# Optimization experiments

Measured on AMD Instinct MI355X. Metric: run time of the kernel, lower is better.

The kernel has to match this reference:

```python
import jax, jax.numpy as jnp
import numpy as np

NEG_SLOPE = 0.2  # PyG GATConv default negative_slope


def gat_conv(x, src, dst, W, a_src, a_dst, bias, concat=True):
    """PyG-style GATConv (self-loops already appended to src/dst).
    x: [N, Fin], W: [Fin, H*C], a_src/a_dst: [H, C], bias: [H*C] or [C].
    """
    N = x.shape[0]
    H, C = a_src.shape
    h = (x @ W).reshape(N, H, C)                       # [N, H, C]
    s_src = jnp.einsum('nhc,hc->nh', h, a_src)         # per-node src logit
    s_dst = jnp.einsum('nhc,hc->nh', h, a_dst)         # per-node dst logit
    e = jax.nn.leaky_relu(s_src[src] + s_dst[dst], NEG_SLOPE)   # [E, H]
    # segment softmax over incoming edges of each destination node
    m = jax.ops.segment_max(e, dst, num_segments=N)    # [N, H]
    ex = jnp.exp(e - m[dst])
    denom = jax.ops.segment_sum(ex, dst, num_segments=N)
    alpha = ex / (denom[dst] + 1e-16)                  # [E, H]
    out = jax.ops.segment_sum(h[src] * alpha[:, :, None], dst, num_segments=N)  # [N,H,C]
    out = out.reshape(N, H * C) if concat else out.mean(axis=1)
    return out + bias


def setup_inputs() -> dict:
    key = jax.random.key(0)
    ks = jax.random.split(key, 12)
    N, E = 20000, 320000
    Fin, Hd, Hh = 384, 256, 4
    x = jax.random.normal(ks[0], (N, Fin), dtype=jnp.float32)
    edge_index = jax.random.randint(ks[1], (2, E), 0, N, dtype=jnp.int32)
    s = lambda k, shp, fan: jax.random.normal(k, shp, dtype=jnp.float32) / np.sqrt(fan)
    return {
        'x': x, 'edge_index': edge_index,
        'W1': s(ks[2], (Fin, Hh * Hd), Fin),
        'a_src1': s(ks[3], (Hh, Hd), Hd), 'a_dst1': s(ks[4], (Hh, Hd), Hd),
        'b1': jnp.zeros((Hh * Hd,), jnp.float32),
        'W2': s(ks[5], (Hh * Hd, Hd), Hh * Hd),
        'a_src2': s(ks[6], (1, Hd), Hd), 'a_dst2': s(ks[7], (1, Hd), Hd),
        'b2': jnp.zeros((Hd,), jnp.float32),
        'Wp1': s(ks[8], (Hd, Hd // 2), Hd), 'bp1': jnp.zeros((Hd // 2,), jnp.float32),
        'Wp2': s(ks[9], (Hd // 2, 1), Hd // 2), 'bp2': jnp.zeros((1,), jnp.float32),
    }


def reference(x, edge_index, W1, a_src1, a_dst1, b1, W2, a_src2, a_dst2, b2,
              Wp1, bp1, Wp2, bp2):
    N = x.shape[0]
    loops = jnp.arange(N, dtype=edge_index.dtype)
    src = jnp.concatenate([edge_index[0], loops])  # PyG add_self_loops=True
    dst = jnp.concatenate([edge_index[1], loops])
    h = jax.nn.elu(gat_conv(x, src, dst, W1, a_src1, a_dst1, b1, concat=True))
    h = jax.nn.elu(gat_conv(h, src, dst, W2, a_src2, a_dst2, b2, concat=True))
    graph_features = jnp.mean(h, axis=0, keepdims=True)  # batch=None path
    infl = jax.nn.sigmoid(jax.nn.relu(h @ Wp1 + bp1) @ Wp2 + bp2)
    return h, graph_features, infl
```

## Files before the change

### kernel.cpp

```cpp
#include <hip/hip_runtime.h>

#define NEG_SLOPE 0.2f
#define SM_SHIFT 3.0f

typedef __bf16 bf16x8 __attribute__((ext_vector_type(8)));
typedef float floatx4 __attribute__((ext_vector_type(4)));
typedef float floatx2 __attribute__((ext_vector_type(2)));
typedef unsigned short ushortx4 __attribute__((ext_vector_type(4)));
typedef unsigned short ushortx8 __attribute__((ext_vector_type(8)));

__device__ __forceinline__ float eluf(float x) { return x > 0.f ? x : __expf(x) - 1.f; }
__device__ __forceinline__ float lrelu(float x) { return x > 0.f ? x : NEG_SLOPE * x; }

__device__ __forceinline__ unsigned short f2bf(float f) {
    unsigned u = __float_as_uint(f);
    u += 0x7FFFu + ((u >> 16) & 1u);
    return (unsigned short)(u >> 16);
}
__device__ __forceinline__ float bf2f(unsigned short h) {
    return __uint_as_float(((unsigned)h) << 16);
}
__device__ __forceinline__ floatx2 mk2(unsigned u) {
    floatx2 r;
    r.x = __uint_as_float(u << 16);
    r.y = __uint_as_float(u & 0xFFFF0000u);
    return r;
}

__device__ __forceinline__ void async16(const unsigned short* g, unsigned short* l) {
    __builtin_amdgcn_global_load_lds(
        (const __attribute__((address_space(1))) unsigned int*)g,
        (__attribute__((address_space(3))) unsigned int*)l,
        16, 0, 0);
}

__global__ __launch_bounds__(256) void prep_kernel(
        const int* __restrict__ ei, int E, int N, int* __restrict__ counts,
        const float* __restrict__ x, unsigned short* __restrict__ xb,
        const float* __restrict__ W1, unsigned short* __restrict__ w1t,
        const float* __restrict__ W2, unsigned short* __restrict__ w2t,
        const float* __restrict__ Wp1, unsigned short* __restrict__ wp1t,
        const float* __restrict__ as1, const float* __restrict__ ad1, float* __restrict__ U) {
    __shared__ float tile[32][33];
    int b = blockIdx.x;
    int t = threadIdx.x;
    int Et = E + N;
    int nA = (Et + 255) >> 8;
    int nB = (N * 96 + 255) >> 8;
    if (b < nA) {
        int i = b * 256 + t;
        if (i < Et) {
            int d = (i < E) ? ei[E + i] : (i - E);
            atomicAdd(&counts[d], 1);
        }
    } else if (b < nA + nB) {
        int i = (b - nA) * 256 + t;
        if (i < N * 96) {
            float4 v = ((const float4*)x)[i];
            ushortx4 o;
            o[0] = f2bf(v.x); o[1] = f2bf(v.y); o[2] = f2bf(v.z); o[3] = f2bf(v.w);
            *(ushortx4*)(xb + (size_t)i * 4) = o;
        }
    } else if (b < nA + nB + 384) {
        int idx = b - nA - nB;
        int n0 = (idx & 31) * 32, k0 = (idx >> 5) * 32;
        int tx = t & 31, ty = t >> 5;
        #pragma unroll
        for (int i = 0; i < 32; i += 8)
            tile[ty + i][tx] = W1[(size_t)(k0 + ty + i) * 1024 + n0 + tx];
        __syncthreads();
        #pragma unroll
        for (int i = 0; i < 32; i += 8)
            w1t[(size_t)(n0 + ty + i) * 384 + k0 + tx] = f2bf(tile[tx][ty + i]);
    } else if (b < nA + nB + 384 + 256) {
        int idx = b - nA - nB - 384;
        int n0 = (idx & 7) * 32, k0 = (idx >> 3) * 32;
        int tx = t & 31, ty = t >> 5;
        #pragma unroll
        for (int i = 0; i < 32; i += 8)
            tile[ty + i][tx] = W2[(size_t)(k0 + ty + i) * 256 + n0 + tx];
        __syncthreads();
        #pragma unroll
        for (int i = 0; i < 32; i += 8)
            w2t[(size_t)(n0 + ty + i) * 1024 + k0 + tx] = f2bf(tile[tx][ty + i]);
    } else if (b < nA + nB + 384 + 256 + 32) {
        int idx = b - nA - nB - 384 - 256;
        int n0 = (idx & 3) * 32, k0 = (idx >> 2) * 32;
        int tx = t & 31, ty = t >> 5;
        #pragma unroll
        for (int i = 0; i < 32; i += 8)
            tile[ty + i][tx] = Wp1[(size_t)(k0 + ty + i) * 128 + n0 + tx];
        __syncthreads();
        #pragma unroll
        for (int i = 0; i < 32; i += 8)
            wp1t[(size_t)(n0 + ty + i) * 256 + k0 + tx] = f2bf(tile[tx][ty + i]);
    } else {
        int idx = b - nA - nB - 384 - 256 - 32;
        int k = idx * 4 + (t >> 6);
        int lane = t & 63;
        #pragma unroll
        for (int r = 0; r < 8; r++) {
            int h = r & 3;
            const float* a = (r < 4 ? as1 : ad1) + h * 256 + lane * 4;
            const float* w = W1 + (size_t)k * 1024 + h * 256 + lane * 4;
            float4 wv = *(const float4*)w;
            float4 av = *(const float4*)a;
            float p = wv.x * av.x + wv.y * av.y + wv.z * av.z + wv.w * av.w;
            #pragma unroll
            for (int off = 32; off; off >>= 1) p += __shfl_xor(p, off);
            if (lane == 0) U[r * 384 + k] = p;
        }
    }
}

__global__ void scan_kernel(int* __restrict__ counts_cursor, int* __restrict__ row_ptr, int N) {
    __shared__ int s_wsum[16];
    __shared__ int s_carry;
    int t = threadIdx.x;
    int lane = t & 63, wid = t >> 6;
    if (t == 0) { s_carry = 0; row_ptr[0] = 0; }
    __syncthreads();
    for (int start = 0; start < N; start += 1024) {
        int i = start + t;
        int v = (i < N) ? counts_cursor[i] : 0;
        int s = v;
        #pragma unroll
        for (int d = 1; d < 64; d <<= 1) {
            int u = __shfl_up(s, d);
            if (lane >= d) s += u;
        }
        if (lane == 63) s_wsum[wid] = s;
        __syncthreads();
        if (wid == 0) {
            int w = (lane < 16) ? s_wsum[lane] : 0;
            #pragma unroll
            for (int d = 1; d < 16; d <<= 1) {
                int u = __shfl_up(w, d);
                if (lane >= d) w += u;
            }
            if (lane < 16) s_wsum[lane] = w;
        }
        __syncthreads();
        int incl = s + (wid ? s_wsum[wid - 1] : 0) + s_carry;
        if (i < N) { row_ptr[i + 1] = incl; counts_cursor[i] = incl - v; }
        __syncthreads();
        if (t == 0) s_carry += s_wsum[15];
        __syncthreads();
    }
}

__global__ void fill_kernel(const int* __restrict__ ei, int E, int N,
                            int* __restrict__ cursor, int* __restrict__ col) {
    int i = blockIdx.x * blockDim.x + threadIdx.x;
    int Et = E + N;
    if (i >= Et) return;
    int s, d;
    if (i < E) { s = ei[i]; d = ei[E + i]; } else { s = d = i - E; }
    int pos = atomicAdd(&cursor[d], 1);
    col[pos] = s;
}

__global__ void sU_kernel(const unsigned short* __restrict__ xb, const float* __restrict__ U,
                          float* __restrict__ ss1, float* __restrict__ sd1, int N) {
    int wid = (blockIdx.x * blockDim.x + threadIdx.x) >> 6;
    int lane = threadIdx.x & 63;
    if (wid >= N) return;
    int half = lane >> 5, l32 = lane & 31;
    int c0 = l32 * 12;
    const unsigned short* row = xb + (size_t)wid * 384 + c0;
    ushortx8 v8 = *(const ushortx8*)row;
    ushortx4 v4 = *(const ushortx4*)(row + 8);
    float xv[12];
    #pragma unroll
    for (int j = 0; j < 8; j++) xv[j] = bf2f(v8[j]);
    #pragma unroll
    for (int j = 0; j < 4; j++) xv[8 + j] = bf2f(v4[j]);
    float p[4];
    #pragma unroll
    for (int r = 0; r < 4; r++) {
        const float* u = U + (half * 4 + r) * 384 + c0;
        float s = 0.f;
        #pragma unroll
        for (int j = 0; j < 12; j++) s += xv[j] * u[j];
        #pragma unroll
        for (int off = 16; off; off >>= 1) s += __shfl_xor(s, off);
        p[r] = s;
    }
    if (l32 == 0) {
        float* dst = half ? (sd1 + wid * 4) : (ss1 + wid * 4);
        dst[0] = p[0]; dst[1] = p[1]; dst[2] = p[2]; dst[3] = p[3];
    }
}

__global__ void s2_kernel(const unsigned short* __restrict__ h2b, const float* __restrict__ a_src,
                          const float* __restrict__ a_dst, float* __restrict__ ssrc,
                          float* __restrict__ sdst, int N) {
    int wid = (blockIdx.x * blockDim.x + threadIdx.x) >> 6;
    int lane = threadIdx.x & 63;
    if (wid >= N) return;
    ushortx4 v = *(const ushortx4*)(h2b + (size_t)wid * 256 + lane * 4);
    float4 a = ((const float4*)a_src)[lane];
    float4 d = ((const float4*)a_dst)[lane];
    float v0 = bf2f(v[0]), v1 = bf2f(v[1]), v2 = bf2f(v[2]), v3 = bf2f(v[3]);
    float s = v0 * a.x + v1 * a.y + v2 * a.z + v3 * a.w;
    float t = v0 * d.x + v1 * d.y + v2 * d.z + v3 * d.w;
    for (int off = 32; off; off >>= 1) { s += __shfl_xor(s, off); t += __shfl_xor(t, off); }
    if (lane == 0) { ssrc[wid] = s; sdst[wid] = t; }
}

__global__ __launch_bounds__(256) void aggx_kernel(const unsigned short* __restrict__ xb,
        const float* __restrict__ ss1, const float* __restrict__ sd1,
        const int* __restrict__ row_ptr, const int* __restrict__ col,
        unsigned short* __restrict__ aggxn, int N) {
    __shared__ unsigned short lds[4][1536];
    __shared__ float pipe[4][72][8];
    int t = threadIdx.x;
    int wv = t >> 6;
    int wid = blockIdx.x * 4 + wv;
    int lane = t & 63;
    bool active = wid < N;
    int half = lane >> 5, l32 = lane & 31;
    int c0 = l32 * 12;
    float4 dsum = {0.f, 0.f, 0.f, 0.f};
    floatx2 acc2[4][6] = {};
    if (active) {
        if (lane < 8) {
            float* pz = &pipe[wv][64 + lane][0];
            #pragma unroll
            for (int j = 0; j < 8; j++) pz[j] = 0.f;
        }
        int base = row_ptr[wid];
        int deg = row_ptr[wid + 1] - base;
        float4 sd = *(const float4*)(sd1 + (size_t)wid * 4);
        for (int chunk = 0; chunk < deg; chunk += 64) {
            int cnt = min(64, deg - chunk);
            int cl = chunk + lane;
            int myO = 0;
            float4 myW = {0.f, 0.f, 0.f, 0.f};
            if (cl < deg) {
                int s = col[base + cl];
                float4 sp = *(const float4*)(ss1 + (size_t)s * 4);
                myW.x = __expf(lrelu(sp.x + sd.x) - SM_SHIFT); dsum.x += myW.x;
                myW.y = __expf(lrelu(sp.y + sd.y) - SM_SHIFT); dsum.y += myW.y;
                myW.z = __expf(lrelu(sp.z + sd.z) - SM_SHIFT); dsum.z += myW.z;
                myW.w = __expf(lrelu(sp.w + sd.w) - SM_SHIFT); dsum.w += myW.w;
                myO = s * 384;
            }
            float* pe = &pipe[wv][lane][0];
            *(float4*)pe = myW;
            pe[4] = __int_as_float(myO);
            int K = (cnt + 1) >> 1;
#define LOADSTG(wS, u4_, u2_, stg) { \
            const float* pq = &pipe[wv][(stg) * 2 + half][0]; \
            wS = *(const float4*)pq; \
            int oN = __float_as_int(pq[4]); \
            const unsigned short* rN = xb + (unsigned)(oN + c0); \
            u4_ = *(const uint4*)rN; u2_ = *(const uint2*)(rN + 8); }
#define CONSUME(cw, u4_, u2_) { \
            floatx2 xv[6]; \
            xv[0] = mk2(u4_.x); xv[1] = mk2(u4_.y); xv[2] = mk2(u4_.z); \
            xv[3] = mk2(u4_.w); xv[4] = mk2(u2_.x); xv[5] = mk2(u2_.y); \
            _Pragma("unroll") for (int j2 = 0; j2 < 6; j2++) { \
                acc2[0][j2] += cw.x * xv[j2]; \
                acc2[1][j2] += cw.y * xv[j2]; \
                acc2[2][j2] += cw.z * xv[j2]; \
                acc2[3][j2] += cw.w * xv[j2]; } }
            float4 wA, wB, wC, wD;
            uint4 uA4, uB4, uC4, uD4;
            uint2 uA2, uB2, uC2, uD2;
            LOADSTG(wA, uA4, uA2, 0)
            LOADSTG(wB, uB4, uB2, 1)
            LOADSTG(wC, uC4, uC2, 2)
            LOADSTG(wD, uD4, uD2, 3)
            int k = 0;
            for (; k + 4 <= K; k += 4) {
                { float4 cw = wA; uint4 u4 = uA4; uint2 u2 = uA2;
                  LOADSTG(wA, uA4, uA2, k + 4) CONSUME(cw, u4, u2) }
                { float4 cw = wB; uint4 u4 = uB4; uint2 u2 = uB2;
                  LOADSTG(wB, uB4, uB2, k + 5) CONSUME(cw, u4, u2) }
                { float4 cw = wC; uint4 u4 = uC4; uint2 u2 = uC2;
                  LOADSTG(wC, uC4, uC2, k + 6) CONSUME(cw, u4, u2) }
                { float4 cw = wD; uint4 u4 = uD4; uint2 u2 = uD2;
                  LOADSTG(wD, uD4, uD2, k + 7) CONSUME(cw, u4, u2) }
            }
            if (k < K)     { CONSUME(wA, uA4, uA2) }
            if (k + 1 < K) { CONSUME(wB, uB4, uB2) }
            if (k + 2 < K) { CONSUME(wC, uC4, uC2) }
#undef LOADSTG
#undef CONSUME
        }
        #pragma unroll
        for (int off = 32; off; off >>= 1) {
            dsum.x += __shfl_xor(dsum.x, off);
            dsum.y += __shfl_xor(dsum.y, off);
            dsum.z += __shfl_xor(dsum.z, off);
            dsum.w += __shfl_xor(dsum.w, off);
        }
        #pragma unroll
        for (int h = 0; h < 4; h++)
            #pragma unroll
            for (int j2 = 0; j2 < 6; j2++) {
                acc2[h][j2].x += __shfl_xor(acc2[h][j2].x, 32);
                acc2[h][j2].y += __shfl_xor(acc2[h][j2].y, 32);
            }
        float dsel0 = half ? dsum.z : dsum.x;
        float dsel1 = half ? dsum.w : dsum.y;
        #pragma unroll
        for (int hh = 0; hh < 2; hh++) {
            int h = half * 2 + hh;
            float dh = hh ? dsel1 : dsel0;
            float inv = 1.f / (dh + 1e-16f);
            ushortx8 o8; ushortx4 o4;
            #pragma unroll
            for (int j = 0; j < 8; j++) {
                float v = half ? acc2[2 + hh][j >> 1][j & 1] : acc2[hh][j >> 1][j & 1];
                o8[j] = f2bf(v * inv);
            }
            #pragma unroll
            for (int j = 0; j < 4; j++) {
                int jj = 8 + j;
                float v = half ? acc2[2 + hh][jj >> 1][jj & 1] : acc2[hh][jj >> 1][jj & 1];
                o4[j] = f2bf(v * inv);
            }
            unsigned short* lp = &lds[wv][h * 384 + c0];
            *(ushortx8*)lp = o8;
            *(ushortx4*)(lp + 8) = o4;
        }
    }
    __syncthreads();
    size_t blockBase = (size_t)blockIdx.x * 4 * 1536;
    const unsigned short* lflat = &lds[0][0];
    #pragma unroll
    for (int j = 0; j < 3; j++) {
        int so = j * 2048 + t * 8;
        int node = blockIdx.x * 4 + so / 1536;
        if (node < N)
            *(ushortx8*)(aggxn + blockBase + so) = *(const ushortx8*)(lflat + so);
    }
}

#define LDK 40

__global__ __launch_bounds__(256) void gemm_l1(const unsigned short* __restrict__ A,
        const unsigned short* __restrict__ Bt, const float* __restrict__ bias,
        unsigned short* __restrict__ Cout, int M) {
    __shared__ unsigned short As[2][128 * 32];
    __shared__ unsigned short Bs[2][128 * 32];
    int t = threadIdx.x;
    int lane = t & 63, wave = t >> 6;
    int wm = (wave >> 1) * 64, wn = (wave & 1) * 64;
    int q = lane >> 4, l16 = lane & 15;
    int row0 = blockIdx.y * 128, col0 = blockIdx.x * 128;
    int hoff = (col0 >> 8) * 384;
    floatx4 acc[4][4] = {};
    int srow = t >> 2, skc = (t & 3) * 8;
    const unsigned short* Ag0 = A + (size_t)min(row0 + srow, M - 1) * 1536 + hoff + skc;
    const unsigned short* Ag1 = A + (size_t)min(row0 + srow + 64, M - 1) * 1536 + hoff + skc;
    const unsigned short* Bg0 = Bt + (size_t)(col0 + srow) * 384 + skc;
    const unsigned short* Bg1 = Bt + (size_t)(col0 + srow + 64) * 384 + skc;
#define STG_L1(buf, kt) \
    async16(Ag0 + (kt), &As[buf][t * 8]); \
    async16(Ag1 + (kt), &As[buf][2048 + t * 8]); \
    async16(Bg0 + (kt), &Bs[buf][t * 8]); \
    async16(Bg1 + (kt), &Bs[buf][2048 + t * 8]);
    STG_L1(0, 0)
    __syncthreads();
    #pragma unroll
    for (int ti = 0; ti < 12; ++ti) {
        int cur = ti & 1;
        if (ti < 11) { STG_L1(cur ^ 1, (ti + 1) * 32) }
        __builtin_amdgcn_sched_barrier(0);
        bf16x8 af[4], bfr[4];
        #pragma unroll
        for (int i = 0; i < 4; i++)
            af[i] = *(const bf16x8*)&As[cur][(wm + i * 16 + l16) * 32 + q * 8];
        #pragma unroll
        for (int j = 0; j < 4; j++)
            bfr[j] = *(const bf16x8*)&Bs[cur][(wn + j * 16 + l16) * 32 + q * 8];
        #pragma unroll
        for (int i = 0; i < 4; i++)
            #pragma unroll
            for (int j = 0; j < 4; j++)
                acc[i][j] = __builtin_amdgcn_mfma_f32_16x16x32_bf16(af[i], bfr[j], acc[i][j], 0, 0, 0);
        __syncthreads();
    }
#undef STG_L1
    float bj[4];
    #pragma unroll
    for (int j = 0; j < 4; j++) bj[j] = bias[col0 + wn + l16 + j * 16];
    #pragma unroll
    for (int i = 0; i < 4; i++) {
        #pragma unroll
        for (int r = 0; r < 4; r++) {
            int grow = row0 + wm + i * 16 + q * 4 + r;
            if (grow < M) {
                unsigned short* cp = Cout + (size_t)grow * 1024 + col0 + wn + l16;
                #pragma unroll
                for (int j = 0; j < 4; j++) cp[j * 16] = f2bf(eluf(acc[i][j][r] + bj[j]));
            }
        }
    }
}

__global__ __launch_bounds__(256) void gemm_l2(const unsigned short* __restrict__ A,
        const unsigned short* __restrict__ Bt, unsigned short* __restrict__ Cout, int M) {
    __shared__ unsigned short As[2][128 * 32];
    __shared__ unsigned short Bs[2][64 * 32];
    int t = threadIdx.x;
    int lane = t & 63, wave = t >> 6;
    int wm = (wave >> 1) * 64, wn = (wave & 1) * 32;
    int q = lane >> 4, l16 = lane & 15;
    int row0 = blockIdx.y * 128, col0 = blockIdx.x * 64;
    floatx4 acc[4][2] = {};
    int srow = t >> 2, skc = (t & 3) * 8;
    const unsigned short* Ag0 = A + (size_t)min(row0 + srow, M - 1) * 1024 + skc;
    const unsigned short* Ag1 = A + (size_t)min(row0 + srow + 64, M - 1) * 1024 + skc;
    const unsigned short* Bg0 = Bt + (size_t)(col0 + srow) * 1024 + skc;
#define STG_L2(buf, kt) \
    async16(Ag0 + (kt), &As[buf][t * 8]); \
    async16(Ag1 + (kt), &As[buf][2048 + t * 8]); \
    async16(Bg0 + (kt), &Bs[buf][t * 8]);
    STG_L2(0, 0)
    __syncthreads();
    #pragma unroll
    for (int ti = 0; ti < 32; ++ti) {
        int cur = ti & 1;
        if (ti < 31) { STG_L2(cur ^ 1, (ti + 1) * 32) }
        __builtin_amdgcn_sched_barrier(0);
        bf16x8 af[4], bfr[2];
        #pragma unroll
        for (int i = 0; i < 4; i++)
            af[i] = *(const bf16x8*)&As[cur][(wm + i * 16 + l16) * 32 + q * 8];
        #pragma unroll
        for (int j = 0; j < 2; j++)
            bfr[j] = *(const bf16x8*)&Bs[cur][(wn + j * 16 + l16) * 32 + q * 8];
        #pragma unroll
        for (int i = 0; i < 4; i++)
            #pragma unroll
            for (int j = 0; j < 2; j++)
                acc[i][j] = __builtin_amdgcn_mfma_f32_16x16x32_bf16(af[i], bfr[j], acc[i][j], 0, 0, 0);
        __syncthreads();
    }
#undef STG_L2
    #pragma unroll
    for (int i = 0; i < 4; i++) {
        #pragma unroll
        for (int r = 0; r < 4; r++) {
            int grow = row0 + wm + i * 16 + q * 4 + r;
            if (grow < M) {
                unsigned short* cp = Cout + (size_t)grow * 256 + col0 + wn + l16;
                #pragma unroll
                for (int j = 0; j < 2; j++) cp[j * 16] = f2bf(acc[i][j][r]);
            }
        }
    }
}

__global__ __launch_bounds__(256) void agg2_kernel(const unsigned short* __restrict__ h2b,
        const float* __restrict__ ss2, const float* __restrict__ sd2,
        const int* __restrict__ row_ptr, const int* __restrict__ col,
        const float* __restrict__ bias, float* __restrict__ out,
        unsigned short* __restrict__ outb, int N) {
    __shared__ float pipe2[4][76][2];
    int t = threadIdx.x;
    int wv = t >> 6;
    int wid = (blockIdx.x * blockDim.x + t) >> 6;
    int lane = t & 63;
    if (wid >= N) return;
    if (lane < 12) {
        pipe2[wv][64 + lane][0] = 0.f;
        pipe2[wv][64 + lane][1] = 0.f;
    }
    int base = row_ptr[wid];
    int deg = row_ptr[wid + 1] - base;
    float sd = sd2[wid];
    floatx2 accA = {0.f, 0.f}, accB = {0.f, 0.f};
    float dsum = 0.f;
    int ch = lane * 4;
    for (int chunk = 0; chunk < deg; chunk += 64) {
        int cnt = min(64, deg - chunk);
        int cl = chunk + lane;
        int myO = 0;
        float myW = 0.f;
        if (cl < deg) {
            int s = col[base + cl];
            myW = __expf(lrelu(ss2[s] + sd) - SM_SHIFT);
            dsum += myW;
            myO = s * 256;
        }
        pipe2[wv][lane][0] = myW;
        pipe2[wv][lane][1] = __int_as_float(myO);
        int K = (cnt + 1) >> 1;
#define LOADSTG2(w0_, w1_, u0_, u1_, stg) { \
        const float* q0 = &pipe2[wv][(stg) * 2][0]; \
        const float* q1 = &pipe2[wv][(stg) * 2 + 1][0]; \
        w0_ = q0[0]; int o0 = __float_as_int(q0[1]); \
        w1_ = q1[0]; int o1 = __float_as_int(q1[1]); \
        u0_ = *(const uint2*)(h2b + (unsigned)(o0 + ch)); \
        u1_ = *(const uint2*)(h2b + (unsigned)(o1 + ch)); }
#define CONSUME2(w0_, w1_, u0_, u1_) { \
        accA += w0_ * mk2(u0_.x); accA += w1_ * mk2(u1_.x); \
        accB += w0_ * mk2(u0_.y); accB += w1_ * mk2(u1_.y); }
        float wa0, wa1, wb0, wb1, wc0, wc1, wd0, wd1, we0, we1, wf0, wf1;
        uint2 ua0, ua1, ub0, ub1, uc0, uc1, ud0, ud1, ue0, ue1, uf0, uf1;
        LOADSTG2(wa0, wa1, ua0, ua1, 0)
        LOADSTG2(wb0, wb1, ub0, ub1, 1)
        LOADSTG2(wc0, wc1, uc0, uc1, 2)
        LOADSTG2(wd0, wd1, ud0, ud1, 3)
        LOADSTG2(we0, we1, ue0, ue1, 4)
        LOADSTG2(wf0, wf1, uf0, uf1, 5)
        int k = 0;
        for (; k + 6 <= K; k += 6) {
            { float p0 = wa0, p1 = wa1; uint2 v0 = ua0, v1 = ua1;
              LOADSTG2(wa0, wa1, ua0, ua1, k + 6) CONSUME2(p0, p1, v0, v1) }
            { float p0 = wb0, p1 = wb1; uint2 v0 = ub0, v1 = ub1;
              LOADSTG2(wb0, wb1, ub0, ub1, k + 7) CONSUME2(p0, p1, v0, v1) }
            { float p0 = wc0, p1 = wc1; uint2 v0 = uc0, v1 = uc1;
              LOADSTG2(wc0, wc1, uc0, uc1, k + 8) CONSUME2(p0, p1, v0, v1) }
            { float p0 = wd0, p1 = wd1; uint2 v0 = ud0, v1 = ud1;
              LOADSTG2(wd0, wd1, ud0, ud1, k + 9) CONSUME2(p0, p1, v0, v1) }
            { float p0 = we0, p1 = we1; uint2 v0 = ue0, v1 = ue1;
              LOADSTG2(we0, we1, ue0, ue1, k + 10) CONSUME2(p0, p1, v0, v1) }
            { float p0 = wf0, p1 = wf1; uint2 v0 = uf0, v1 = uf1;
              LOADSTG2(wf0, wf1, uf0, uf1, k + 11) CONSUME2(p0, p1, v0, v1) }
        }
        if (k < K)     { CONSUME2(wa0, wa1, ua0, ua1) }
        if (k + 1 < K) { CONSUME2(wb0, wb1, ub0, ub1) }
        if (k + 2 < K) { CONSUME2(wc0, wc1, uc0, uc1) }
        if (k + 3 < K) { CONSUME2(wd0, wd1, ud0, ud1) }
        if (k + 4 < K) { CONSUME2(we0, we1, ue0, ue1) }
#undef LOADSTG2
#undef CONSUME2
    }
    #pragma unroll
    for (int off = 32; off; off >>= 1) dsum += __shfl_xor(dsum, off);
    float inv = 1.f / (dsum + 1e-16f);
    float4 o;
    o.x = eluf(accA.x * inv + bias[ch + 0]);
    o.y = eluf(accA.y * inv + bias[ch + 1]);
    o.z = eluf(accB.x * inv + bias[ch + 2]);
    o.w = eluf(accB.y * inv + bias[ch + 3]);
    *(float4*)(out + (size_t)wid * 256 + ch) = o;
    ushortx4 ob;
    ob[0] = f2bf(o.x); ob[1] = f2bf(o.y); ob[2] = f2bf(o.z); ob[3] = f2bf(o.w);
    *(ushortx4*)(outb + (size_t)wid * 256 + ch) = ob;
}

__global__ __launch_bounds__(256) void tail_kernel(const float* __restrict__ h,
        const unsigned short* __restrict__ hbf, const unsigned short* __restrict__ wp1t,
        const float* __restrict__ bp1, const float* __restrict__ Wp2,
        const float* __restrict__ bp2, float* __restrict__ gf, float* __restrict__ infl, int M) {
    int b = blockIdx.x;
    int nInfl = (M + 127) / 128;
    if (b < nInfl) {
        __shared__ unsigned short As[128 * LDK];
        __shared__ unsigned short Bs[128 * LDK];
        __shared__ float partial[2][128];
        int t = threadIdx.x;
        int lane = t & 63, wave = t >> 6;
        int wm = (wave >> 1) * 64, wn = (wave & 1) * 64;
        int q = lane >> 4, l16 = lane & 15;
        int row0 = b * 128;
        floatx4 acc[4][4] = {};
        int sg = (t & 7) * 4;
        int sr = t >> 3;
        for (int kt = 0; kt < 256; kt += 32) {
            #pragma unroll
            for (int p = 0; p < 4; p++) {
                int r = sr + p * 32;
                int ga = min(row0 + r, M - 1);
                *(ushortx4*)&As[r * LDK + sg] = *(const ushortx4*)(hbf + (size_t)ga * 256 + kt + sg);
                *(ushortx4*)&Bs[r * LDK + sg] = *(const ushortx4*)(wp1t + (size_t)r * 256 + kt + sg);
            }
            __syncthreads();
            bf16x8 af[4], bfr[4];
            #pragma unroll
            for (int i = 0; i < 4; i++)
                af[i] = *(const bf16x8*)&As[(wm + i * 16 + l16) * LDK + q * 8];
            #pragma unroll
            for (int j = 0; j < 4; j++)
                bfr[j] = *(const bf16x8*)&Bs[(wn + j * 16 + l16) * LDK + q * 8];
            #pragma unroll
            for (int i = 0; i < 4; i++)
                #pragma unroll
                for (int j = 0; j < 4; j++)
                    acc[i][j] = __builtin_amdgcn_mfma_f32_16x16x32_bf16(af[i], bfr[j], acc[i][j], 0, 0, 0);
            __syncthreads();
        }
        float b1v[4], w2v[4];
        #pragma unroll
        for (int j = 0; j < 4; j++) {
            int colj = wn + j * 16 + l16;
            b1v[j] = bp1[colj];
            w2v[j] = Wp2[colj];
        }
        #pragma unroll
        for (int i = 0; i < 4; i++) {
            #pragma unroll
            for (int r = 0; r < 4; r++) {
                float s = fmaxf(acc[i][0][r] + b1v[0], 0.f) * w2v[0]
                        + fmaxf(acc[i][1][r] + b1v[1], 0.f) * w2v[1]
                        + fmaxf(acc[i][2][r] + b1v[2], 0.f) * w2v[2]
                        + fmaxf(acc[i][3][r] + b1v[3], 0.f) * w2v[3];
                #pragma unroll
                for (int off = 1; off < 16; off <<= 1) s += __shfl_xor(s, off);
                if (l16 == 0) partial[wave & 1][wm + i * 16 + q * 4 + r] = s;
            }
        }
        __syncthreads();
        if (t < 128) {
            int row = row0 + t;
            if (row < M) {
                float v = partial[0][t] + partial[1][t] + bp2[0];
                infl[row] = 1.f / (1.f + __expf(-v));
            }
        }
    } else {
        int bb = b - nInfl;
        int c = threadIdx.x;
        int per = (M + 159) / 160;
        int n0 = bb * per;
        int n1 = min(M, n0 + per);
        float a0 = 0.f, a1 = 0.f, a2 = 0.f, a3 = 0.f;
        float a4 = 0.f, a5 = 0.f, a6 = 0.f, a7 = 0.f;
        int n = n0;
        for (; n + 8 <= n1; n += 8) {
            a0 += h[(size_t)(n + 0) * 256 + c];
            a1 += h[(size_t)(n + 1) * 256 + c];
            a2 += h[(size_t)(n + 2) * 256 + c];
            a3 += h[(size_t)(n + 3) * 256 + c];
            a4 += h[(size_t)(n + 4) * 256 + c];
            a5 += h[(size_t)(n + 5) * 256 + c];
            a6 += h[(size_t)(n + 6) * 256 + c];
            a7 += h[(size_t)(n + 7) * 256 + c];
        }
        for (; n < n1; n++) a0 += h[(size_t)n * 256 + c];
        float acc = ((a0 + a1) + (a2 + a3)) + ((a4 + a5) + (a6 + a7));
        atomicAdd(&gf[c], acc * (1.0f / M));
    }
}

extern "C" void kernel_launch(void* const* d_in, const int* in_sizes, int n_in,
                              void* d_out, int out_size, void* d_ws, size_t ws_size,
                              hipStream_t stream) {
    const float* x   = (const float*)d_in[0];
    const int*   ei  = (const int*)d_in[1];
    const float* W1  = (const float*)d_in[2];
    const float* as1 = (const float*)d_in[3];
    const float* ad1 = (const float*)d_in[4];
    const float* b1  = (const float*)d_in[5];
    const float* W2  = (const float*)d_in[6];
    const float* as2 = (const float*)d_in[7];
    const float* ad2 = (const float*)d_in[8];
    const float* b2  = (const float*)d_in[9];
    const float* Wp1 = (const float*)d_in[10];
    const float* bp1 = (const float*)d_in[11];
    const float* Wp2 = (const float*)d_in[12];
    const float* bp2 = (const float*)d_in[13];

    const int N  = in_sizes[0] / 384;
    const int E  = in_sizes[1] / 2;
    const int Et = E + N;

    char* wsp = (char*)d_ws;
    unsigned short* xb    = (unsigned short*)wsp; wsp += (size_t)N * 384  * sizeof(short);
    unsigned short* aggxn = (unsigned short*)wsp; wsp += (size_t)N * 1536 * sizeof(short);
    unsigned short* h1eb  = (unsigned short*)wsp; wsp += (size_t)N * 1024 * sizeof(short);
    unsigned short* h2b   = (unsigned short*)wsp; wsp += (size_t)N * 256  * sizeof(short);
    unsigned short* hbf   = (unsigned short*)wsp; wsp += (size_t)N * 256  * sizeof(short);
    unsigned short* w1t   = (unsigned short*)wsp; wsp += (size_t)1024 * 384 * sizeof(short);
    unsigned short* w2t   = (unsigned short*)wsp; wsp += (size_t)256 * 1024 * sizeof(short);
    unsigned short* wp1t  = (unsigned short*)wsp; wsp += (size_t)128 * 256 * sizeof(short);
    float* U   = (float*)wsp; wsp += (size_t)8 * 384 * sizeof(float);
    float* ss1 = (float*)wsp; wsp += (size_t)N * 4 * sizeof(float);
    float* sd1 = (float*)wsp; wsp += (size_t)N * 4 * sizeof(float);
    float* ss2 = (float*)wsp; wsp += (size_t)N * sizeof(float);
    float* sd2 = (float*)wsp; wsp += (size_t)N * sizeof(float);
    int* row_ptr = (int*)wsp; wsp += (size_t)(N + 1) * sizeof(int);
    int* cursor  = (int*)wsp; wsp += (size_t)N * sizeof(int);
    int* col     = (int*)wsp;

    float* out_h  = (float*)d_out;
    float* out_gf = out_h + (size_t)N * 256;
    float* out_if = out_gf + 256;

    hipMemsetAsync(cursor, 0, (size_t)N * sizeof(int), stream);
    int nA = (Et + 255) / 256;
    int nB = (N * 96 + 255) / 256;
    int nPrep = nA + nB + 384 + 256 + 32 + 96;
    prep_kernel<<<nPrep, 256, 0, stream>>>(ei, E, N, cursor, x, xb, W1, w1t, W2, w2t, Wp1, wp1t, as1, ad1, U);
    scan_kernel<<<1, 1024, 0, stream>>>(cursor, row_ptr, N);
    fill_kernel<<<nA, 256, 0, stream>>>(ei, E, N, cursor, col);

    sU_kernel<<<(N + 3) / 4, 256, 0, stream>>>(xb, U, ss1, sd1, N);
    aggx_kernel<<<(N + 3) / 4, 256, 0, stream>>>(xb, ss1, sd1, row_ptr, col, aggxn, N);
    gemm_l1<<<dim3(8, (N + 127) / 128), 256, 0, stream>>>(aggxn, w1t, b1, h1eb, N);

    gemm_l2<<<dim3(4, (N + 127) / 128), 256, 0, stream>>>(h1eb, w2t, h2b, N);
    s2_kernel<<<(N + 3) / 4, 256, 0, stream>>>(h2b, as2, ad2, ss2, sd2, N);
    agg2_kernel<<<(N + 3) / 4, 256, 0, stream>>>(h2b, ss2, sd2, row_ptr, col, b2, out_h, hbf, N);

    hipMemsetAsync(out_gf, 0, 256 * sizeof(float), stream);
    tail_kernel<<<(N + 127) / 128 + 160, 256, 0, stream>>>(out_h, hbf, wp1t, bp1, Wp2, bp2, out_gf, out_if, N);
}
```

Baseline: 338.9 us.

## Fuse fill with sU, fold s2 logits into gemm_l2 epilogue, single-pass scan

Replaces the looped block scan with a single pass where each thread scans 20 counts serially. Merges the CSR fill and layer-1 logit kernels into one launch, and computes the layer-2 src/dst logits inside the gemm_l2 epilogue via shuffle reductions and atomics (with an added memset). The graph-mean reduction now reads the bf16 copy of h instead of fp32. This reduces launches and memory traffic. The scan now caps N at 20480 and the mean uses bf16-rounded values.

```diff
diff --git a/kernel.cpp b/kernel.cpp
--- a/kernel.cpp
+++ b/kernel.cpp
@@ -113,99 +113,97 @@
     }
 }
 
+#define SCAN_PER 20
 __global__ void scan_kernel(int* __restrict__ counts_cursor, int* __restrict__ row_ptr, int N) {
     __shared__ int s_wsum[16];
-    __shared__ int s_carry;
     int t = threadIdx.x;
     int lane = t & 63, wid = t >> 6;
-    if (t == 0) { s_carry = 0; row_ptr[0] = 0; }
+    int i0 = t * SCAN_PER;
+    int v[SCAN_PER];
+    int lsum = 0;
+    #pragma unroll
+    for (int j = 0; j < SCAN_PER; j++) {
+        int i = i0 + j;
+        int x = (i < N) ? counts_cursor[i] : 0;
+        v[j] = lsum;
+        lsum += x;
+    }
+    int s = lsum;
+    #pragma unroll
+    for (int d = 1; d < 64; d <<= 1) {
+        int u = __shfl_up(s, d);
+        if (lane >= d) s += u;
+    }
+    if (lane == 63) s_wsum[wid] = s;
     __syncthreads();
-    for (int start = 0; start < N; start += 1024) {
-        int i = start + t;
-        int v = (i < N) ? counts_cursor[i] : 0;
-        int s = v;
-        #pragma unroll
-        for (int d = 1; d < 64; d <<= 1) {
-            int u = __shfl_up(s, d);
-            if (lane >= d) s += u;
-        }
-        if (lane == 63) s_wsum[wid] = s;
-        __syncthreads();
-        if (wid == 0) {
-            int w = (lane < 16) ? s_wsum[lane] : 0;
-            #pragma unroll
-            for (int d = 1; d < 16; d <<= 1) {
-                int u = __shfl_up(w, d);
-                if (lane >= d) w += u;
-            }
-            if (lane < 16) s_wsum[lane] = w;
-        }
-        __syncthreads();
-        int incl = s + (wid ? s_wsum[wid - 1] : 0) + s_carry;
-        if (i < N) { row_ptr[i + 1] = incl; counts_cursor[i] = incl - v; }
-        __syncthreads();
-        if (t == 0) s_carry += s_wsum[15];
-        __syncthreads();
-    }
-}
-
-__global__ void fill_kernel(const int* __restrict__ ei, int E, int N,
-                            int* __restrict__ cursor, int* __restrict__ col) {
-    int i = blockIdx.x * blockDim.x + threadIdx.x;
+    if (wid == 0 && lane < 16) {
+        int w = s_wsum[lane];
+        #pragma unroll
+        for (int d = 1; d < 16; d <<= 1) {
+            int u = __shfl_up(w, d);
+            if (lane >= d) w += u;
+        }
+        s_wsum[lane] = w;
+    }
+    __syncthreads();
+    int base = s - lsum + (wid ? s_wsum[wid - 1] : 0);
+    if (t == 0) row_ptr[0] = 0;
+    #pragma unroll
+    for (int j = 0; j < SCAN_PER; j++) {
+        int i = i0 + j;
+        if (i < N) {
+            int excl = base + v[j];
+            int incl = base + ((j + 1 < SCAN_PER) ? v[j + 1] : lsum);
+            counts_cursor[i] = excl;
+            row_ptr[i + 1] = incl;
+        }
+    }
+}
+
+__global__ __launch_bounds__(256) void fill_sU_kernel(const int* __restrict__ ei, int E, int N,
+        int* __restrict__ cursor, int* __restrict__ col,
+        const unsigned short* __restrict__ xb, const float* __restrict__ U,
+        float* __restrict__ ss1, float* __restrict__ sd1) {
+    int b = blockIdx.x;
     int Et = E + N;
-    if (i >= Et) return;
-    int s, d;
-    if (i < E) { s = ei[i]; d = ei[E + i]; } else { s = d = i - E; }
-    int pos = atomicAdd(&cursor[d], 1);
-    col[pos] = s;
-}
-
-__global__ void sU_kernel(const unsigned short* __restrict__ xb, const float* __restrict__ U,
-                          float* __restrict__ ss1, float* __restrict__ sd1, int N) {
-    int wid = (blockIdx.x * blockDim.x + threadIdx.x) >> 6;
-    int lane = threadIdx.x & 63;
-    if (wid >= N) return;
-    int half = lane >> 5, l32 = lane & 31;
-    int c0 = l32 * 12;
-    const unsigned short* row = xb + (size_t)wid * 384 + c0;
-    ushortx8 v8 = *(const ushortx8*)row;
-    ushortx4 v4 = *(const ushortx4*)(row + 8);
-    float xv[12];
-    #pragma unroll
-    for (int j = 0; j < 8; j++) xv[j] = bf2f(v8[j]);
-    #pragma unroll
-    for (int j = 0; j < 4; j++) xv[8 + j] = bf2f(v4[j]);
-    float p[4];
-    #pragma unroll
-    for (int r = 0; r < 4; r++) {
-        const float* u = U + (half * 4 + r) * 384 + c0;
-        float s = 0.f;
-        #pragma unroll
-        for (int j = 0; j < 12; j++) s += xv[j] * u[j];
-        #pragma unroll
-        for (int off = 16; off; off >>= 1) s += __shfl_xor(s, off);
-        p[r] = s;
-    }
-    if (l32 == 0) {
-        float* dst = half ? (sd1 + wid * 4) : (ss1 + wid * 4);
-        dst[0] = p[0]; dst[1] = p[1]; dst[2] = p[2]; dst[3] = p[3];
-    }
-}
-
-__global__ void s2_kernel(const unsigned short* __restrict__ h2b, const float* __restrict__ a_src,
-                          const float* __restrict__ a_dst, float* __restrict__ ssrc,
-                          float* __restrict__ sdst, int N) {
-    int wid = (blockIdx.x * blockDim.x + threadIdx.x) >> 6;
-    int lane = threadIdx.x & 63;
-    if (wid >= N) return;
-    ushortx4 v = *(const ushortx4*)(h2b + (size_t)wid * 256 + lane * 4);
-    float4 a = ((const float4*)a_src)[lane];
-    float4 d = ((const float4*)a_dst)[lane];
-    float v0 = bf2f(v[0]), v1 = bf2f(v[1]), v2 = bf2f(v[2]), v3 = bf2f(v[3]);
-    float s = v0 * a.x + v1 * a.y + v2 * a.z + v3 * a.w;
-    float t = v0 * d.x + v1 * d.y + v2 * d.z + v3 * d.w;
-    for (int off = 32; off; off >>= 1) { s += __shfl_xor(s, off); t += __shfl_xor(t, off); }
-    if (lane == 0) { ssrc[wid] = s; sdst[wid] = t; }
+    int nF = (Et + 255) >> 8;
+    if (b < nF) {
+        int i = b * 256 + threadIdx.x;
+        if (i >= Et) return;
+        int s, d;
+        if (i < E) { s = ei[i]; d = ei[E + i]; } else { s = d = i - E; }
+        int pos = atomicAdd(&cursor[d], 1);
+        col[pos] = s;
+    } else {
+        int wid = ((b - nF) * 256 + threadIdx.x) >> 6;
+        int lane = threadIdx.x & 63;
+        if (wid >= N) return;
+        int half = lane >> 5, l32 = lane & 31;
+        int c0 = l32 * 12;
+        const unsigned short* row = xb + (size_t)wid * 384 + c0;
+        ushortx8 v8 = *(const ushortx8*)row;
+        ushortx4 v4 = *(const ushortx4*)(row + 8);
+        float xv[12];
+        #pragma unroll
+        for (int j = 0; j < 8; j++) xv[j] = bf2f(v8[j]);
+        #pragma unroll
+        for (int j = 0; j < 4; j++) xv[8 + j] = bf2f(v4[j]);
+        float p[4];
+        #pragma unroll
+        for (int r = 0; r < 4; r++) {
+            const float* u = U + (half * 4 + r) * 384 + c0;
+            float s = 0.f;
+            #pragma unroll
+            for (int j = 0; j < 12; j++) s += xv[j] * u[j];
+            #pragma unroll
+            for (int off = 16; off; off >>= 1) s += __shfl_xor(s, off);
+            p[r] = s;
+        }
+        if (l32 == 0) {
+            float* dst = half ? (sd1 + wid * 4) : (ss1 + wid * 4);
+            dst[0] = p[0]; dst[1] = p[1]; dst[2] = p[2]; dst[3] = p[3];
+        }
+    }
 }
 
 __global__ __launch_bounds__(256) void aggx_kernel(const unsigned short* __restrict__ xb,
@@ -403,7 +401,9 @@
 }
 
 __global__ __launch_bounds__(256) void gemm_l2(const unsigned short* __restrict__ A,
-        const unsigned short* __restrict__ Bt, unsigned short* __restrict__ Cout, int M) {
+        const unsigned short* __restrict__ Bt, const float* __restrict__ as2,
+        const float* __restrict__ ad2, unsigned short* __restrict__ Cout,
+        float* __restrict__ ssrc, float* __restrict__ sdst, int M) {
     __shared__ unsigned short As[2][128 * 32];
     __shared__ unsigned short Bs[2][64 * 32];
     int t = threadIdx.x;
@@ -442,15 +442,33 @@
         __syncthreads();
     }
 #undef STG_L2
+    float as2v[2], ad2v[2];
+    #pragma unroll
+    for (int j = 0; j < 2; j++) {
+        int colj = col0 + wn + l16 + j * 16;
+        as2v[j] = as2[colj];
+        ad2v[j] = ad2[colj];
+    }
     #pragma unroll
     for (int i = 0; i < 4; i++) {
         #pragma unroll
         for (int r = 0; r < 4; r++) {
             int grow = row0 + wm + i * 16 + q * 4 + r;
+            float ps = acc[i][0][r] * as2v[0] + acc[i][1][r] * as2v[1];
+            float pt = acc[i][0][r] * ad2v[0] + acc[i][1][r] * ad2v[1];
+            #pragma unroll
+            for (int off = 1; off < 16; off <<= 1) {
+                ps += __shfl_xor(ps, off);
+                pt += __shfl_xor(pt, off);
+            }
             if (grow < M) {
                 unsigned short* cp = Cout + (size_t)grow * 256 + col0 + wn + l16;
                 #pragma unroll
                 for (int j = 0; j < 2; j++) cp[j * 16] = f2bf(acc[i][j][r]);
+                if (l16 == 0) {
+                    atomicAdd(&ssrc[grow], ps);
+                    atomicAdd(&sdst[grow], pt);
+                }
             }
         }
     }
@@ -546,7 +564,7 @@
     *(ushortx4*)(outb + (size_t)wid * 256 + ch) = ob;
 }
 
-__global__ __launch_bounds__(256) void tail_kernel(const float* __restrict__ h,
+__global__ __launch_bounds__(256) void tail_kernel(
         const unsigned short* __restrict__ hbf, const unsigned short* __restrict__ wp1t,
         const float* __restrict__ bp1, const float* __restrict__ Wp2,
         const float* __restrict__ bp2, float* __restrict__ gf, float* __restrict__ infl, int M) {
@@ -625,16 +643,16 @@
         float a4 = 0.f, a5 = 0.f, a6 = 0.f, a7 = 0.f;
         int n = n0;
         for (; n + 8 <= n1; n += 8) {
-            a0 += h[(size_t)(n + 0) * 256 + c];
-            a1 += h[(size_t)(n + 1) * 256 + c];
-            a2 += h[(size_t)(n + 2) * 256 + c];
-            a3 += h[(size_t)(n + 3) * 256 + c];
-            a4 += h[(size_t)(n + 4) * 256 + c];
-            a5 += h[(size_t)(n + 5) * 256 + c];
-            a6 += h[(size_t)(n + 6) * 256 + c];
-            a7 += h[(size_t)(n + 7) * 256 + c];
-        }
-        for (; n < n1; n++) a0 += h[(size_t)n * 256 + c];
+            a0 += bf2f(hbf[(size_t)(n + 0) * 256 + c]);
+            a1 += bf2f(hbf[(size_t)(n + 1) * 256 + c]);
+            a2 += bf2f(hbf[(size_t)(n + 2) * 256 + c]);
+            a3 += bf2f(hbf[(size_t)(n + 3) * 256 + c]);
+            a4 += bf2f(hbf[(size_t)(n + 4) * 256 + c]);
+            a5 += bf2f(hbf[(size_t)(n + 5) * 256 + c]);
+            a6 += bf2f(hbf[(size_t)(n + 6) * 256 + c]);
+            a7 += bf2f(hbf[(size_t)(n + 7) * 256 + c]);
+        }
+        for (; n < n1; n++) a0 += bf2f(hbf[(size_t)n * 256 + c]);
         float acc = ((a0 + a1) + (a2 + a3)) + ((a4 + a5) + (a6 + a7));
         atomicAdd(&gf[c], acc * (1.0f / M));
     }
@@ -690,16 +708,15 @@
     int nPrep = nA + nB + 384 + 256 + 32 + 96;
     prep_kernel<<<nPrep, 256, 0, stream>>>(ei, E, N, cursor, x, xb, W1, w1t, W2, w2t, Wp1, wp1t, as1, ad1, U);
     scan_kernel<<<1, 1024, 0, stream>>>(cursor, row_ptr, N);
-    fill_kernel<<<nA, 256, 0, stream>>>(ei, E, N, cursor, col);
-
-    sU_kernel<<<(N + 3) / 4, 256, 0, stream>>>(xb, U, ss1, sd1, N);
+    fill_sU_kernel<<<nA + (N + 3) / 4, 256, 0, stream>>>(ei, E, N, cursor, col, xb, U, ss1, sd1);
+
     aggx_kernel<<<(N + 3) / 4, 256, 0, stream>>>(xb, ss1, sd1, row_ptr, col, aggxn, N);
     gemm_l1<<<dim3(8, (N + 127) / 128), 256, 0, stream>>>(aggxn, w1t, b1, h1eb, N);
 
-    gemm_l2<<<dim3(4, (N + 127) / 128), 256, 0, stream>>>(h1eb, w2t, h2b, N);
-    s2_kernel<<<(N + 3) / 4, 256, 0, stream>>>(h2b, as2, ad2, ss2, sd2, N);
+    hipMemsetAsync(ss2, 0, (size_t)2 * N * sizeof(float), stream);
+    gemm_l2<<<dim3(4, (N + 127) / 128), 256, 0, stream>>>(h1eb, w2t, as2, ad2, h2b, ss2, sd2, N);
     agg2_kernel<<<(N + 3) / 4, 256, 0, stream>>>(h2b, ss2, sd2, row_ptr, col, b2, out_h, hbf, N);
 
     hipMemsetAsync(out_gf, 0, 256 * sizeof(float), stream);
-    tail_kernel<<<(N + 127) / 128 + 160, 256, 0, stream>>>(out_h, hbf, wp1t, bp1, Wp2, bp2, out_gf, out_if, N);
-}
+    tail_kernel<<<(N + 127) / 128 + 160, 256, 0, stream>>>(hbf, wp1t, bp1, Wp2, bp2, out_gf, out_if, N);
+}
```

After: 339.2 us. Within noise of the previous version (+0.1%).
